# Optimization experiments

Hardware: AMD Instinct MI355X
Metric: run time of the kernel (lower is better)

The kernel has to match this reference:

```python
import jax, jax.numpy as jnp
import numpy as np

SEQ, B, N_IN, H, L = 8192, 1, 64, 1024, 5


def leaky_relu(x):
    return jnp.where(x >= 0, x, 0.01 * x)  # torch LeakyReLU default slope 0.01


def setup_inputs() -> dict:
    key = jax.random.key(0)
    ks = jax.random.split(key, 6)
    s_in = 1.0 / np.sqrt(N_IN)
    s_h = 1.0 / np.sqrt(H)
    return {
        "data_in": jax.random.normal(ks[0], (SEQ, B, N_IN), jnp.float32),
        "w1": jax.random.normal(ks[1], (H, N_IN), jnp.float32) * s_in,
        "b1": jnp.zeros((H,), jnp.float32),
        "W_ih": jax.random.normal(ks[2], (L, 4 * H, H), jnp.float32) * s_h,
        "W_hh": jax.random.normal(ks[3], (L, 4 * H, H), jnp.float32) * s_h,
        "b_ih": jnp.zeros((L, 4 * H), jnp.float32),
        "b_hh": jnp.zeros((L, 4 * H), jnp.float32),
        "w2": jax.random.normal(ks[4], (N_IN, H), jnp.float32) * s_h,
        "b2": jnp.zeros((N_IN,), jnp.float32),
        "h0": jnp.zeros((L, B, H), jnp.float32),
        "c0": jnp.zeros((L, B, H), jnp.float32),
    }


def _lstm_layer(x, h0, c0, Wih, Whh, b):
    # x: (SEQ, B, H_in); h0, c0: (B, H); Wih: (4H, H_in); Whh: (4H, H); b: (4H,)
    def step(carry, x_t):
        h, c = carry
        z = x_t @ Wih.T + h @ Whh.T + b  # (B, 4H)
        i, f, g, o = jnp.split(z, 4, axis=-1)  # torch gate order i,f,g,o
        i = jax.nn.sigmoid(i)
        f = jax.nn.sigmoid(f)
        g = jnp.tanh(g)
        o = jax.nn.sigmoid(o)
        c = f * c + i * g
        h = o * jnp.tanh(c)
        return (h, c), h

    (_, _), hs = jax.lax.scan(step, (h0, c0), x)
    return hs  # (SEQ, B, H)


def reference(data_in, w1, b1, W_ih, W_hh, b_ih, b_hh, w2, b2, h0, c0):
    out = leaky_relu(data_in @ w1.T + b1)  # (SEQ, B, H)
    for l in range(W_ih.shape[0]):  # stacked LSTM, layers is a static small int
        out = _lstm_layer(out, h0[l], c0[l], W_ih[l], W_hh[l], b_ih[l] + b_hh[l])
    out = leaky_relu(out)
    return jnp.tanh(out @ w2.T + b2)  # (SEQ, B, N_IN)
```

## Files before the change

### kernel.cpp

```cpp
#include <hip/hip_runtime.h>
#include <stdint.h>

typedef unsigned int  u32;
typedef unsigned short u16;

#define SEQ    8192
#define HID    1024
#define NL     5
#define NWG    256
#define TPB    256
#define PAIRS  20
#define RPW    20
#define NVR    12
#define NLR    8
#define WSTEPS (SEQ + NL - 1)
#define LWGS   52
#define RING   8

#define WS_X0    ((size_t)0)
#define WS_H5    ((size_t)16*1024*1024)
#define WS_SLOT  ((size_t)32*1024*1024)
#define WS_SYNC  (WS_SLOT + (size_t)128*1024)
#define WS_NEED  (WS_SYNC + 4096)

__device__ __forceinline__ float bf2f(u16 v) { return __uint_as_float(((u32)v) << 16); }
__device__ __forceinline__ float bflo(u32 v) { return __uint_as_float(v << 16); }
__device__ __forceinline__ float bfhi(u32 v) { return __uint_as_float(v & 0xffff0000u); }

__device__ __forceinline__ u16 f2bf(float f) {
  u32 u = __float_as_uint(f);
  u32 r = u + 0x7fffu + ((u >> 16) & 1u);
  return (u16)(r >> 16);
}
__device__ __forceinline__ float lrelu(float x) { return (x >= 0.f) ? x : 0.01f * x; }
__device__ __forceinline__ float sigm(float x)  { return 1.f / (1.f + __expf(-x)); }
__device__ __forceinline__ float tanh_f(float x) {
  float e = __expf(-2.f * fabsf(x));
  float t = (1.f - e) / (1.f + e);
  return (x >= 0.f) ? t : -t;
}

__device__ __forceinline__ float dot2bf(u32 w, u32 v, float acc) {
  return fmaf(bfhi(w), bfhi(v), fmaf(bflo(w), bflo(v), acc));
}

#if defined(__has_builtin)
#if __has_builtin(__builtin_amdgcn_fdot2_f32_bf16)
#define HAS_DOT2 1
typedef __bf16 bf16x2 __attribute__((ext_vector_type(2)));
__device__ __forceinline__ float hwdot2(u32 a, u32 b, float c) {
  union U { u32 u; bf16x2 v; };
  U x, y; x.u = a; y.u = b;
  return __builtin_amdgcn_fdot2_f32_bf16(x.v, y.v, c, false);
}
#endif
#endif
#ifndef HAS_DOT2
#define HAS_DOT2 0
__device__ __forceinline__ float hwdot2(u32 a, u32 b, float c) { return dot2bf(a, b, c); }
#endif

__device__ __forceinline__ u32 agent_load(const u32* p) {
  return __hip_atomic_load((u32*)p, __ATOMIC_RELAXED, __HIP_MEMORY_SCOPE_AGENT);
}
__device__ __forceinline__ void agent_store(u32* p, u32 v) {
  __hip_atomic_store(p, v, __ATOMIC_RELAXED, __HIP_MEMORY_SCOPE_AGENT);
}

__device__ __forceinline__ void rel_drain() {
  asm volatile("s_waitcnt vmcnt(0)" ::: "memory");
}

__device__ __forceinline__ int first_wg(int l) { return (l << 10) / PAIRS; }

__global__ void k_detect(const u32* __restrict__ w1, u32* __restrict__ flag) {
  int lane = threadIdx.x;
  int cnt = 0;
#pragma unroll
  for (int i = 0; i < 4; ++i) {
    u32 w = w1[lane * 4 + i];
    u32 e = (w >> 23) & 0xffu;
    cnt += (e >= 100u && e <= 140u) ? 1 : 0;
  }
  cnt += __shfl_xor(cnt, 32); cnt += __shfl_xor(cnt, 16); cnt += __shfl_xor(cnt, 8);
  cnt += __shfl_xor(cnt, 4);  cnt += __shfl_xor(cnt, 2);  cnt += __shfl_xor(cnt, 1);
  if (lane == 0) {
    u32 f = (cnt > 128) ? 1u : 0u;
#if HAS_DOT2
    u32 a1 = (u32)f2bf(1.5f)   | ((u32)f2bf(-2.25f) << 16);
    u32 b1v = (u32)f2bf(0.5f)  | ((u32)f2bf(4.0f)   << 16);
    u32 a2 = (u32)f2bf(0.125f) | ((u32)f2bf(3.0f)   << 16);
    u32 b2v = (u32)f2bf(8.0f)  | ((u32)f2bf(-0.5f)  << 16);
    float t1 = hwdot2(a1, b1v, 1.0f);
    float t2 = hwdot2(a2, b2v, 0.5f);
    if (fabsf(t1 + 7.25f) < 1e-2f && fabsf(t2) < 1e-2f) f |= 2u;
#endif
    *flag = f;
  }
}

__global__ void __launch_bounds__(256) k_in(const void* __restrict__ din,
                                            const void* __restrict__ w1,
                                            const void* __restrict__ b1,
                                            u32* __restrict__ X0,
                                            const u32* __restrict__ flagp) {
  const u32 isf = *flagp & 1u;
  int t = blockIdx.x, tid = threadIdx.x;
  __shared__ float xs[64];
  if (isf) {
    if (tid < 64) xs[tid] = ((const float*)din)[(size_t)t * 64 + tid];
  } else {
    if (tid < 32) {
      u32 v = ((const u32*)din)[(size_t)t * 32 + tid];
      xs[2 * tid] = bflo(v); xs[2 * tid + 1] = bfhi(v);
    }
  }
  __syncthreads();
  float o[4];
#pragma unroll
  for (int r = 0; r < 4; ++r) {
    int i = tid * 4 + r;
    float a = 0.f;
    if (isf) {
      const float* wr = (const float*)w1 + (size_t)i * 64;
#pragma unroll
      for (int d = 0; d < 64; ++d) a = fmaf(wr[d], xs[d], a);
      a += ((const float*)b1)[i];
    } else {
      const u32* wr = (const u32*)w1 + (size_t)i * 32;
#pragma unroll
      for (int d = 0; d < 32; ++d) {
        u32 w = wr[d];
        a = fmaf(bflo(w), xs[2 * d], a);
        a = fmaf(bfhi(w), xs[2 * d + 1], a);
      }
      a += bf2f(((const u16*)b1)[i]);
    }
    o[r] = lrelu(a);
  }
  X0[(size_t)t * 512 + tid * 2]     = (u32)f2bf(o[0]) | ((u32)f2bf(o[1]) << 16);
  X0[(size_t)t * 512 + tid * 2 + 1] = (u32)f2bf(o[2]) | ((u32)f2bf(o[3]) << 16);
}

__global__ void __launch_bounds__(TPB, 1) k_wave(const void* __restrict__ WihP,
                                                 const void* __restrict__ WhhP,
                                                 const void* __restrict__ bihP,
                                                 const void* __restrict__ bhhP,
                                                 const void* __restrict__ h0P,
                                                 const void* __restrict__ c0P,
                                                 const u32* __restrict__ X0,
                                                 u32* __restrict__ H5,
                                                 u32* slots, u32* flags,
                                                 const u32* __restrict__ flagp) {
  const u32 dfl = *flagp;
  const u32 isf = dfl & 1u;
  const bool ud2 = (dfl & 2u) != 0u;
  const int tid  = threadIdx.x;
  const int lane = tid & 63;
  const int wv   = tid >> 6;
  const int wg   = blockIdx.x;

  __shared__ u32   vlds[2][64 * 17];
  __shared__ u32   wlds[4 * NLR * 1024];
  __shared__ float zrow[80];

  u32 W[NVR][16];
#pragma unroll
  for (int i = 0; i < RPW; ++i) {
    int rr = wv * RPW + i;
    int p = rr >> 2, q = rr & 3;
    int g = wg * PAIRS + p;
    int lg = g >> 10, j = g & 1023;
    u32 tmp[16];
    if (isf) {
      const float* matf = (lane < 32) ? (const float*)WihP : (const float*)WhhP;
      const float4* s4 = (const float4*)(matf + ((size_t)(lg * 4096 + q * 1024 + j)) * 1024 + (lane & 31) * 32);
#pragma unroll
      for (int q4 = 0; q4 < 8; ++q4) {
        float4 f = s4[q4];
        tmp[q4 * 2]     = (u32)f2bf(f.x) | ((u32)f2bf(f.y) << 16);
        tmp[q4 * 2 + 1] = (u32)f2bf(f.z) | ((u32)f2bf(f.w) << 16);
      }
    } else {
      const u32* mat = (lane < 32) ? (const u32*)WihP : (const u32*)WhhP;
      const uint4* s4 = (const uint4*)(mat + ((size_t)(lg * 4096 + q * 1024 + j)) * 512 + (lane & 31) * 16);
      uint4 a0 = s4[0], a1 = s4[1], a2 = s4[2], a3 = s4[3];
      tmp[0]=a0.x; tmp[1]=a0.y; tmp[2]=a0.z;  tmp[3]=a0.w;
      tmp[4]=a1.x; tmp[5]=a1.y; tmp[6]=a1.z;  tmp[7]=a1.w;
      tmp[8]=a2.x; tmp[9]=a2.y; tmp[10]=a2.z; tmp[11]=a2.w;
      tmp[12]=a3.x;tmp[13]=a3.y;tmp[14]=a3.z; tmp[15]=a3.w;
    }
    if (i < NVR) {
#pragma unroll
      for (int d = 0; d < 16; ++d) W[i][d] = tmp[d];
    } else {
      u32* base = &wlds[(wv * NLR + (i - NVR)) * 1024];
#pragma unroll
      for (int d4 = 0; d4 < 4; ++d4) {
        uint4 v4 = make_uint4(tmp[d4*4], tmp[d4*4+1], tmp[d4*4+2], tmp[d4*4+3]);
        *(uint4*)&base[d4 * 256 + lane * 4] = v4;
      }
    }
  }

  float cst = 0.f;
  float b0 = 0.f, b1g = 0.f, b2g = 0.f, b3g = 0.f;
  if (wv == 0 && lane < PAIRS) {
    int g = wg * PAIRS + lane, lg = g >> 10, j = g & 1023;
    cst = isf ? ((const float*)c0P)[lg * 1024 + j] : bf2f(((const u16*)c0P)[lg * 1024 + j]);
#pragma unroll
    for (int q = 0; q < 4; ++q) {
      int r = lg * 4096 + q * 1024 + j;
      float bb = isf ? (((const float*)bihP)[r] + ((const float*)bhhP)[r])
                     : (bf2f(((const u16*)bihP)[r]) + bf2f(((const u16*)bhhP)[r]));
      if (q == 0) b0 = bb; else if (q == 1) b1g = bb; else if (q == 2) b2g = bb; else b3g = bb;
    }
  }
  if (tid < PAIRS / 2) {
    int g = wg * PAIRS + 2 * tid, lg = g >> 10, j = g & 1023;
    u32 v;
    if (isf) {
      const float* h0f = (const float*)h0P;
      v = (u32)f2bf(h0f[lg * 1024 + j]) | ((u32)f2bf(h0f[lg * 1024 + j + 1]) << 16);
    } else {
      const u16* h0b = (const u16*)h0P;
      v = (u32)h0b[lg * 1024 + j] | ((u32)h0b[lg * 1024 + j + 1] << 16);
    }
    agent_store(&slots[(size_t)(lg * RING + 7) * 512 + (j >> 1)], v);
  }

  const int l_lo = (wg * PAIRS) >> 10;
  const int l_hi = (wg * PAIRS + PAIRS - 1) >> 10;
  const int mlo = (l_lo > 0) ? l_lo - 1 : 0;
  const bool haswar = (l_hi + 1) < NL;
  const int f_lo = first_wg(l_lo), f_hi = first_wg(l_hi);

  __threadfence();
  __syncthreads();
  if (tid == 0) {
    agent_store(&flags[l_lo * 64 + (wg - f_lo)], 1u);
    if (l_hi != l_lo) agent_store(&flags[l_hi * 64 + (wg - f_hi)], 1u);
  }

  int budget = 20000000;

  for (int s = 0; s < WSTEPS; ++s) {
    if (wv == 0) {
      u32 need = (u32)(s + 1);
      for (;;) {
        u32 mn = 0xFFFFFFFFu;
        if (lane < LWGS) {
          for (int m = mlo; m <= l_hi; ++m) {
            u32 v = agent_load(&flags[m * 64 + lane]);
            mn = (v < mn) ? v : mn;
          }
          if (haswar) {
            u32 v = agent_load(&flags[(l_hi + 1) * 64 + lane]) + (u32)(RING - 2);
            mn = (v < mn) ? v : mn;
          }
        }
        u32 o;
        o = (u32)__shfl_xor((int)mn, 32); mn = (o < mn) ? o : mn;
        o = (u32)__shfl_xor((int)mn, 16); mn = (o < mn) ? o : mn;
        o = (u32)__shfl_xor((int)mn, 8);  mn = (o < mn) ? o : mn;
        o = (u32)__shfl_xor((int)mn, 4);  mn = (o < mn) ? o : mn;
        o = (u32)__shfl_xor((int)mn, 2);  mn = (o < mn) ? o : mn;
        o = (u32)__shfl_xor((int)mn, 1);  mn = (o < mn) ? o : mn;
        if (mn >= need) break;
        if (--budget < 0) break;
      }
    }
    __syncthreads();

#pragma unroll
    for (int sel = 0; sel < 2; ++sel) {
      int L = l_lo + sel;
      if (L <= l_hi) {
        int t = s - L;
        if (t >= 0 && t < SEQ) {
          const u32* hsrc = slots + (size_t)(L * RING + ((t - 1) & 7)) * 512;
          const u32* xsrc = (L == 0) ? (X0 + (size_t)t * 512)
                                     : (slots + (size_t)((L - 1) * RING + (t & 7)) * 512);
#pragma unroll
          for (int rr2 = 0; rr2 < 4; ++rr2) {
            int gidx = tid + rr2 * 256;
            u32 val;
            if (gidx < 512) val = (L == 0) ? xsrc[gidx] : agent_load(&xsrc[gidx]);
            else            val = agent_load(&hsrc[gidx - 512]);
            vlds[sel][(gidx >> 4) * 17 + (gidx & 15)] = val;
          }
        }
      }
    }
    __syncthreads();

    {
      int curl = -1;
      u32 vreg[16];
#pragma unroll
      for (int i = 0; i < RPW; ++i) {
        int rr = wv * RPW + i;
        int p = rr >> 2;
        int g = wg * PAIRS + p;
        int lg = g >> 10;
        int t = s - lg;
        if (t >= 0 && t < SEQ) {
          if (lg != curl) {
            curl = lg;
            const u32* vb = &vlds[lg - l_lo][lane * 17];
#pragma unroll
            for (int d = 0; d < 16; ++d) vreg[d] = vb[d];
          }
          float a0 = 0.f, a1 = 0.f, a2 = 0.f, a3 = 0.f;
          if (i < NVR) {
            if (ud2) {
#pragma unroll
              for (int d = 0; d < 16; d += 4) {
                a0 = hwdot2(W[i][d],   vreg[d],   a0);
                a1 = hwdot2(W[i][d+1], vreg[d+1], a1);
                a2 = hwdot2(W[i][d+2], vreg[d+2], a2);
                a3 = hwdot2(W[i][d+3], vreg[d+3], a3);
              }
            } else {
#pragma unroll
              for (int d = 0; d < 16; d += 4) {
                a0 = fmaf(bflo(W[i][d]),   bflo(vreg[d]),   a0);
                a0 = fmaf(bfhi(W[i][d]),   bfhi(vreg[d]),   a0);
                a1 = fmaf(bflo(W[i][d+1]), bflo(vreg[d+1]), a1);
                a1 = fmaf(bfhi(W[i][d+1]), bfhi(vreg[d+1]), a1);
                a2 = fmaf(bflo(W[i][d+2]), bflo(vreg[d+2]), a2);
                a2 = fmaf(bfhi(W[i][d+2]), bfhi(vreg[d+2]), a2);
                a3 = fmaf(bflo(W[i][d+3]), bflo(vreg[d+3]), a3);
                a3 = fmaf(bfhi(W[i][d+3]), bfhi(vreg[d+3]), a3);
              }
            }
          } else {
            const uint4* wl = (const uint4*)&wlds[(wv * NLR + (i - NVR)) * 1024 + lane * 4];
#pragma unroll
            for (int d4 = 0; d4 < 4; ++d4) {
              uint4 w4 = wl[d4 * 64];
              if (ud2) {
                a0 = hwdot2(w4.x, vreg[d4*4+0], a0);
                a1 = hwdot2(w4.y, vreg[d4*4+1], a1);
                a2 = hwdot2(w4.z, vreg[d4*4+2], a2);
                a3 = hwdot2(w4.w, vreg[d4*4+3], a3);
              } else {
                a0 = fmaf(bflo(w4.x), bflo(vreg[d4*4+0]), a0);
                a0 = fmaf(bfhi(w4.x), bfhi(vreg[d4*4+0]), a0);
                a1 = fmaf(bflo(w4.y), bflo(vreg[d4*4+1]), a1);
                a1 = fmaf(bfhi(w4.y), bfhi(vreg[d4*4+1]), a1);
                a2 = fmaf(bflo(w4.z), bflo(vreg[d4*4+2]), a2);
                a2 = fmaf(bfhi(w4.z), bfhi(vreg[d4*4+2]), a2);
                a3 = fmaf(bflo(w4.w), bflo(vreg[d4*4+3]), a3);
                a3 = fmaf(bfhi(w4.w), bfhi(vreg[d4*4+3]), a3);
              }
            }
          }
          float r = (a0 + a1) + (a2 + a3);
          r += __shfl_xor(r, 32);
          r += __shfl_xor(r, 16);
          r += __shfl_xor(r, 8);
          r += __shfl_xor(r, 4);
          r += __shfl_xor(r, 2);
          r += __shfl_xor(r, 1);
          if (lane == 0) zrow[rr] = r;
        }
      }
    }
    __syncthreads();

    if (wv == 0) {
      u16 hb = 0;
      int g = wg * PAIRS + lane;
      int lg = g >> 10;
      int t = s - lg;
      bool act = (lane < PAIRS) && (t >= 0) && (t < SEQ);
      if (act) {
        float zi = zrow[lane * 4 + 0] + b0;
        float zf = zrow[lane * 4 + 1] + b1g;
        float zg = zrow[lane * 4 + 2] + b2g;
        float zo = zrow[lane * 4 + 3] + b3g;
        float ig = sigm(zi), fg = sigm(zf), gg = tanh_f(zg), og = sigm(zo);
        float c = fg * cst + ig * gg;
        cst = c;
        hb = f2bf(og * tanh_f(c));
      }
      u16 hnb = (u16)__shfl_xor((int)hb, 1);
      if (act && ((lane & 1) == 0)) {
        int j = g & 1023;
        u32 v = (u32)hb | ((u32)hnb << 16);
        agent_store(&slots[(size_t)(lg * RING + (t & 7)) * 512 + (j >> 1)], v);
        if (lg == NL - 1) H5[(size_t)t * 512 + (j >> 1)] = v;
      }
      rel_drain();
      if (lane == 0) {
        agent_store(&flags[l_lo * 64 + (wg - f_lo)], (u32)(s + 2));
        if (l_hi != l_lo) agent_store(&flags[l_hi * 64 + (wg - f_hi)], (u32)(s + 2));
      }
    }
  }
}

__global__ void __launch_bounds__(256) k_out(const u32* __restrict__ H5,
                                             const void* __restrict__ w2,
                                             const void* __restrict__ b2,
                                             void* __restrict__ out,
                                             const u32* __restrict__ flagp) {
  const u32 isf = *flagp & 1u;
  int t = blockIdx.x, tid = threadIdx.x;
  __shared__ float hs[1024];
  __shared__ float part[256];
#pragma unroll
  for (int r = 0; r < 2; ++r) {
    int idx = tid + r * 256;
    u32 v = H5[(size_t)t * 512 + idx];
    hs[2 * idx]     = lrelu(bflo(v));
    hs[2 * idx + 1] = lrelu(bfhi(v));
  }
  __syncthreads();
  int n = tid & 63, qq = tid >> 6;
  float a = 0.f;
  if (isf) {
    const float* wr = (const float*)w2 + (size_t)n * 1024 + qq * 256;
    const float* hb = &hs[qq * 256];
#pragma unroll
    for (int d = 0; d < 256; ++d) a = fmaf(wr[d], hb[d], a);
  } else {
    const u32* wr = (const u32*)w2 + (size_t)n * 512 + qq * 128;
    const float* hb = &hs[qq * 256];
#pragma unroll
    for (int d = 0; d < 128; ++d) {
      u32 w = wr[d];
      a = fmaf(bflo(w), hb[2 * d], a);
      a = fmaf(bfhi(w), hb[2 * d + 1], a);
    }
  }
  part[tid] = a;
  __syncthreads();
  if (tid < 64) {
    float bb = isf ? ((const float*)b2)[tid] : bf2f(((const u16*)b2)[tid]);
    float y = part[tid] + part[tid + 64] + part[tid + 128] + part[tid + 192] + bb;
    float r = tanh_f(y);
    if (isf) ((float*)out)[(size_t)t * 64 + tid] = r;
    else     ((u16*)out)[(size_t)t * 64 + tid] = f2bf(r);
  }
}

extern "C" void kernel_launch(void* const* d_in, const int* in_sizes, int n_in,
                              void* d_out, int out_size, void* d_ws, size_t ws_size,
                              hipStream_t stream) {
  (void)in_sizes; (void)n_in; (void)out_size;
  if (ws_size < WS_NEED) return;

  const void* din = d_in[0];
  const void* w1  = d_in[1];
  const void* b1  = d_in[2];
  const void* Wih = d_in[3];
  const void* Whh = d_in[4];
  const void* bih = d_in[5];
  const void* bhh = d_in[6];
  const void* w2  = d_in[7];
  const void* b2  = d_in[8];
  const void* h0  = d_in[9];
  const void* c0  = d_in[10];

  char* ws = (char*)d_ws;
  u32* X0    = (u32*)(ws + WS_X0);
  u32* H5    = (u32*)(ws + WS_H5);
  u32* slot  = (u32*)(ws + WS_SLOT);
  u32* flags = (u32*)(ws + WS_SYNC);
  u32* dflag = (u32*)(ws + WS_SYNC + 2048);

  hipMemsetAsync(flags, 0, 4096, stream);
  k_detect<<<1, 64, 0, stream>>>((const u32*)w1, dflag);
  k_in  <<<SEQ, 256, 0, stream>>>(din, w1, b1, X0, dflag);
  k_wave<<<NWG, TPB, 0, stream>>>(Wih, Whh, bih, bhh, h0, c0, X0, H5, slot, flags, dflag);
  k_out <<<SEQ, 256, 0, stream>>>(H5, w2, b2, d_out, dflag);
}
```

Measured before the change: 116.4 ms.

## Replace flag-based step sync with sequence-tagged data chunks in LSTM wavefront

Hidden-state ring slots now hold per-workgroup 16-word chunks, each 4-word group carrying a timestep tag next to three data words. Consumers poll the tags of the chunks they need instead of a separate flag array. This removes the separate flag store, the vmcnt drain and the flag-then-data round trip on every step. Stores go out as dwordx4 with sc0 sc1 so each tag and its data arrive together at the last-level cache. The cost is index arithmetic (divide by ten, padding) in the gather, wider polling loads, and a write-after-read flag that is still kept for ring reuse.

```diff
diff --git a/kernel.cpp b/kernel.cpp
--- a/kernel.cpp
+++ b/kernel.cpp
@@ -16,11 +16,13 @@
 #define WSTEPS (SEQ + NL - 1)
 #define LWGS   52
 #define RING   8
+#define CHW    16
+#define SSTR   (LWGS * CHW)
 
 #define WS_X0    ((size_t)0)
 #define WS_H5    ((size_t)16*1024*1024)
 #define WS_SLOT  ((size_t)32*1024*1024)
-#define WS_SYNC  (WS_SLOT + (size_t)128*1024)
+#define WS_SYNC  (WS_SLOT + (size_t)192*1024)
 #define WS_NEED  (WS_SYNC + 4096)
 
 __device__ __forceinline__ float bf2f(u16 v) { return __uint_as_float(((u32)v) << 16); }
@@ -63,15 +65,19 @@
 __device__ __forceinline__ u32 agent_load(const u32* p) {
   return __hip_atomic_load((u32*)p, __ATOMIC_RELAXED, __HIP_MEMORY_SCOPE_AGENT);
 }
-__device__ __forceinline__ void agent_store(u32* p, u32 v) {
-  __hip_atomic_store(p, v, __ATOMIC_RELAXED, __HIP_MEMORY_SCOPE_AGENT);
-}
-
-__device__ __forceinline__ void rel_drain() {
-  asm volatile("s_waitcnt vmcnt(0)" ::: "memory");
+
+__device__ __forceinline__ void llc_store(u32* p, u32 v) {
+  asm volatile("global_store_dword %0, %1, off sc0 sc1" : : "v"(p), "v"(v) : "memory");
+}
+
+typedef u32 u32x4_t __attribute__((ext_vector_type(4)));
+__device__ __forceinline__ void llc_store4(u32* p, u32 tag, u32 a, u32 b, u32 c) {
+  u32x4_t q; q.x = tag; q.y = a; q.z = b; q.w = c;
+  asm volatile("global_store_dwordx4 %0, %1, off sc0 sc1" : : "v"(p), "v"(q) : "memory");
 }
 
 __device__ __forceinline__ int first_wg(int l) { return (l << 10) / PAIRS; }
+
 
 __global__ void k_detect(const u32* __restrict__ w1, u32* __restrict__ flag) {
   int lane = threadIdx.x;
@@ -216,57 +222,78 @@
       if (q == 0) b0 = bb; else if (q == 1) b1g = bb; else if (q == 2) b2g = bb; else b3g = bb;
     }
   }
-  if (tid < PAIRS / 2) {
-    int g = wg * PAIRS + 2 * tid, lg = g >> 10, j = g & 1023;
-    u32 v;
-    if (isf) {
-      const float* h0f = (const float*)h0P;
-      v = (u32)f2bf(h0f[lg * 1024 + j]) | ((u32)f2bf(h0f[lg * 1024 + j + 1]) << 16);
-    } else {
-      const u16* h0b = (const u16*)h0P;
-      v = (u32)h0b[lg * 1024 + j] | ((u32)h0b[lg * 1024 + j + 1] << 16);
-    }
-    agent_store(&slots[(size_t)(lg * RING + 7) * 512 + (j >> 1)], v);
-  }
 
   const int l_lo = (wg * PAIRS) >> 10;
   const int l_hi = (wg * PAIRS + PAIRS - 1) >> 10;
-  const int mlo = (l_lo > 0) ? l_lo - 1 : 0;
-  const bool haswar = (l_hi + 1) < NL;
+  const bool span = (l_hi != l_lo);
   const int f_lo = first_wg(l_lo), f_hi = first_wg(l_hi);
-
-  __threadfence();
+  const int c_lo = wg - f_lo, c_hi = wg - f_hi;
+
+  if (wv == 0) {
+    int g = wg * PAIRS + lane;
+    int lg = g >> 10, j = g & 1023;
+    u32 hv = 0;
+    if ((lane < PAIRS) && !(lane & 1)) {
+      if (isf) {
+        const float* h0f = (const float*)h0P;
+        hv = (u32)f2bf(h0f[lg * 1024 + j]) | ((u32)f2bf(h0f[lg * 1024 + j + 1]) << 16);
+      } else {
+        const u16* h0b = (const u16*)h0P;
+        hv = (u32)h0b[lg * 1024 + j] | ((u32)h0b[lg * 1024 + j + 1] << 16);
+      }
+    }
+    u32 ga = (u32)__shfl((int)hv, 6 * (lane & 3));
+    u32 gb = (u32)__shfl((int)hv, 6 * (lane & 3) + 2);
+    u32 gc = (u32)__shfl((int)hv, 6 * (lane & 3) + 4);
+#pragma unroll
+    for (int sel = 0; sel < 2; ++sel) {
+      int L = l_lo + sel;
+      if (L <= l_hi) {
+        int cc = (sel == 0) ? c_lo : c_hi;
+        u32* cb = slots + (L * RING + 7) * SSTR + cc * CHW;
+        if (lane < 4) llc_store4(cb + lane * 4, 0xFFFFFFFFu, ga, gb, gc);
+      }
+    }
+  }
   __syncthreads();
-  if (tid == 0) {
-    agent_store(&flags[l_lo * 64 + (wg - f_lo)], 1u);
-    if (l_hi != l_lo) agent_store(&flags[l_hi * 64 + (wg - f_hi)], 1u);
-  }
 
   int budget = 20000000;
 
   for (int s = 0; s < WSTEPS; ++s) {
+    const int t0 = s - l_lo;
+    const int t1 = s - l_hi;
+    if (t1 >= SEQ) break;
+    const bool p0 = (t0 >= 0) && (t0 < SEQ);
+    const bool p1 = span && (t1 >= 0);
+
     if (wv == 0) {
-      u32 need = (u32)(s + 1);
+      const u32 need = (u32)(s + 1);
+      const int lc = lane * CHW;
+      const u32 *tA = 0, *tXA = 0, *tB = 0, *tXB = 0, *wf1 = 0, *wf2 = 0;
+      u32 eA = 0, eXA = 0, eB = 0, eXB = 0;
+      if (p0) { tA = slots + (l_lo * RING + ((t0 - 1) & 7)) * SSTR + lc; eA = (u32)(t0 - 1); }
+      if (p0 && l_lo > 0) { tXA = slots + ((l_lo - 1) * RING + (t0 & 7)) * SSTR + lc; eXA = (u32)t0; }
+      if (p1) {
+        tB  = slots + (l_hi * RING + ((t1 - 1) & 7)) * SSTR + lc; eB  = (u32)(t1 - 1);
+        tXB = slots + (l_lo * RING + (t1 & 7)) * SSTR + lc;       eXB = (u32)t1;
+      }
+      if (p0 && (l_lo + 1) < NL)         wf1 = flags + (l_lo + 1) * 64 + lane;
+      if (span && p1 && (l_hi + 1) < NL) wf2 = flags + (l_hi + 1) * 64 + lane;
       for (;;) {
-        u32 mn = 0xFFFFFFFFu;
+        bool pass = true;
         if (lane < LWGS) {
-          for (int m = mlo; m <= l_hi; ++m) {
-            u32 v = agent_load(&flags[m * 64 + lane]);
-            mn = (v < mn) ? v : mn;
-          }
-          if (haswar) {
-            u32 v = agent_load(&flags[(l_hi + 1) * 64 + lane]) + (u32)(RING - 2);
-            mn = (v < mn) ? v : mn;
-          }
+          if (tA)  pass = pass & (agent_load(tA)  == eA)  & (agent_load(tA + 4)  == eA)
+                               & (agent_load(tA + 8)  == eA)  & (agent_load(tA + 12)  == eA);
+          if (tXA) pass = pass & (agent_load(tXA) == eXA) & (agent_load(tXA + 4) == eXA)
+                               & (agent_load(tXA + 8) == eXA) & (agent_load(tXA + 12) == eXA);
+          if (tB)  pass = pass & (agent_load(tB)  == eB)  & (agent_load(tB + 4)  == eB)
+                               & (agent_load(tB + 8)  == eB)  & (agent_load(tB + 12)  == eB);
+          if (tXB) pass = pass & (agent_load(tXB) == eXB) & (agent_load(tXB + 4) == eXB)
+                               & (agent_load(tXB + 8) == eXB) & (agent_load(tXB + 12) == eXB);
+          if (wf1) pass = pass & ((agent_load(wf1) + (u32)(RING - 2)) >= need);
+          if (wf2) pass = pass & ((agent_load(wf2) + (u32)(RING - 2)) >= need);
         }
-        u32 o;
-        o = (u32)__shfl_xor((int)mn, 32); mn = (o < mn) ? o : mn;
-        o = (u32)__shfl_xor((int)mn, 16); mn = (o < mn) ? o : mn;
-        o = (u32)__shfl_xor((int)mn, 8);  mn = (o < mn) ? o : mn;
-        o = (u32)__shfl_xor((int)mn, 4);  mn = (o < mn) ? o : mn;
-        o = (u32)__shfl_xor((int)mn, 2);  mn = (o < mn) ? o : mn;
-        o = (u32)__shfl_xor((int)mn, 1);  mn = (o < mn) ? o : mn;
-        if (mn >= need) break;
+        if (__all(pass)) break;
         if (--budget < 0) break;
       }
     }
@@ -278,15 +305,29 @@
       if (L <= l_hi) {
         int t = s - L;
         if (t >= 0 && t < SEQ) {
-          const u32* hsrc = slots + (size_t)(L * RING + ((t - 1) & 7)) * 512;
-          const u32* xsrc = (L == 0) ? (X0 + (size_t)t * 512)
-                                     : (slots + (size_t)((L - 1) * RING + (t & 7)) * 512);
 #pragma unroll
           for (int rr2 = 0; rr2 < 4; ++rr2) {
             int gidx = tid + rr2 * 256;
             u32 val;
-            if (gidx < 512) val = (L == 0) ? xsrc[gidx] : agent_load(&xsrc[gidx]);
-            else            val = agent_load(&hsrc[gidx - 512]);
+            if (gidx < 512) {
+              if (L == 0) {
+                val = X0[(size_t)t * 512 + gidx];
+              } else {
+                int qp = (L - 1) * 512 + gidx;
+                int wsrc = (qp * 6554) >> 16;
+                int qq = qp - wsrc * 10;
+                int word = 1 + qq + ((qq * 11) >> 5);
+                val = agent_load(slots + ((L - 1) * RING + (t & 7)) * SSTR
+                                 + (wsrc - first_wg(L - 1)) * CHW + word);
+              }
+            } else {
+              int qp = L * 512 + (gidx - 512);
+              int wsrc = (qp * 6554) >> 16;
+              int qq = qp - wsrc * 10;
+              int word = 1 + qq + ((qq * 11) >> 5);
+              val = agent_load(slots + (L * RING + ((t - 1) & 7)) * SSTR
+                               + (wsrc - first_wg(L)) * CHW + word);
+            }
             vlds[sel][(gidx >> 4) * 17 + (gidx & 15)] = val;
           }
         }
@@ -373,8 +414,8 @@
       u16 hb = 0;
       int g = wg * PAIRS + lane;
       int lg = g >> 10;
-      int t = s - lg;
-      bool act = (lane < PAIRS) && (t >= 0) && (t < SEQ);
+      int tg = s - lg;
+      bool act = (lane < PAIRS) && (tg >= 0) && (tg < SEQ);
       if (act) {
         float zi = zrow[lane * 4 + 0] + b0;
         float zf = zrow[lane * 4 + 1] + b1g;
@@ -386,16 +427,27 @@
         hb = f2bf(og * tanh_f(c));
       }
       u16 hnb = (u16)__shfl_xor((int)hb, 1);
-      if (act && ((lane & 1) == 0)) {
-        int j = g & 1023;
-        u32 v = (u32)hb | ((u32)hnb << 16);
-        agent_store(&slots[(size_t)(lg * RING + (t & 7)) * 512 + (j >> 1)], v);
-        if (lg == NL - 1) H5[(size_t)t * 512 + (j >> 1)] = v;
-      }
-      rel_drain();
+      u32 v = (u32)hb | ((u32)hnb << 16);
+      u32 ga = (u32)__shfl((int)v, 6 * (lane & 3));
+      u32 gb = (u32)__shfl((int)v, 6 * (lane & 3) + 2);
+      u32 gc = (u32)__shfl((int)v, 6 * (lane & 3) + 4);
+#pragma unroll
+      for (int sel = 0; sel < 2; ++sel) {
+        int L = l_lo + sel;
+        if (L <= l_hi) {
+          int tL = s - L;
+          if (tL >= 0 && tL < SEQ) {
+            int cc = (sel == 0) ? c_lo : c_hi;
+            u32* cb = slots + (L * RING + (tL & 7)) * SSTR + cc * CHW;
+            if (lane < 4) llc_store4(cb + lane * 4, (u32)tL, ga, gb, gc);
+            if (act && !(lane & 1) && (lg == L) && (L == NL - 1))
+              H5[(size_t)tL * 512 + ((g & 1023) >> 1)] = v;
+          }
+        }
+      }
       if (lane == 0) {
-        agent_store(&flags[l_lo * 64 + (wg - f_lo)], (u32)(s + 2));
-        if (l_hi != l_lo) agent_store(&flags[l_hi * 64 + (wg - f_hi)], (u32)(s + 2));
+        if (l_lo > 0) llc_store(flags + l_lo * 64 + c_lo, (u32)(s + 2));
+        if (span)     llc_store(flags + l_hi * 64 + c_hi, (u32)(s + 2));
       }
     }
   }
```

Result: slower. 127.0 ms (+9.1%).

## Replace flag-polling barrier with sequence-tagged slots and per-layer epoch counters

Applied to the files above, without the earlier changes.

Each hidden-state slot entry becomes a 64-bit word holding the bf16 pair and its timestep tag, so consumers spin directly on the data until the tags match. This replaces the per-step min-reduction over all producer flags and the vmcnt drain before publishing. Write-after-read safety now uses per-layer atomic epoch counters, checked only against the next layer, and the ring is deepened to 16 slots. The slot area doubles in size and epoch updates are contended atomics, and correctness depends on 64-bit atomic stores landing as one unit.

```diff
diff --git a/kernel.cpp b/kernel.cpp
--- a/kernel.cpp
+++ b/kernel.cpp
@@ -3,6 +3,7 @@
 
 typedef unsigned int  u32;
 typedef unsigned short u16;
+typedef unsigned long long u64;
 
 #define SEQ    8192
 #define HID    1024
@@ -15,12 +16,12 @@
 #define NLR    8
 #define WSTEPS (SEQ + NL - 1)
 #define LWGS   52
-#define RING   8
+#define RING   16
 
 #define WS_X0    ((size_t)0)
 #define WS_H5    ((size_t)16*1024*1024)
 #define WS_SLOT  ((size_t)32*1024*1024)
-#define WS_SYNC  (WS_SLOT + (size_t)128*1024)
+#define WS_SYNC  (WS_SLOT + (size_t)384*1024)
 #define WS_NEED  (WS_SYNC + 4096)
 
 __device__ __forceinline__ float bf2f(u16 v) { return __uint_as_float(((u32)v) << 16); }
@@ -63,15 +64,15 @@
 __device__ __forceinline__ u32 agent_load(const u32* p) {
   return __hip_atomic_load((u32*)p, __ATOMIC_RELAXED, __HIP_MEMORY_SCOPE_AGENT);
 }
-__device__ __forceinline__ void agent_store(u32* p, u32 v) {
+__device__ __forceinline__ u64 slot_load(const u64* p) {
+  return __hip_atomic_load((u64*)p, __ATOMIC_RELAXED, __HIP_MEMORY_SCOPE_AGENT);
+}
+__device__ __forceinline__ void slot_store(u64* p, u64 v) {
   __hip_atomic_store(p, v, __ATOMIC_RELAXED, __HIP_MEMORY_SCOPE_AGENT);
 }
-
-__device__ __forceinline__ void rel_drain() {
-  asm volatile("s_waitcnt vmcnt(0)" ::: "memory");
-}
-
-__device__ __forceinline__ int first_wg(int l) { return (l << 10) / PAIRS; }
+__device__ __forceinline__ void epoch_add(u32* p) {
+  (void)__hip_atomic_fetch_add(p, 1u, __ATOMIC_RELAXED, __HIP_MEMORY_SCOPE_AGENT);
+}
 
 __global__ void k_detect(const u32* __restrict__ w1, u32* __restrict__ flag) {
   int lane = threadIdx.x;
@@ -150,7 +151,7 @@
                                                  const void* __restrict__ c0P,
                                                  const u32* __restrict__ X0,
                                                  u32* __restrict__ H5,
-                                                 u32* slots, u32* flags,
+                                                 u64* slots64, u32* epochs,
                                                  const u32* __restrict__ flagp) {
   const u32 dfl = *flagp;
   const u32 isf = dfl & 1u;
@@ -226,68 +227,55 @@
       const u16* h0b = (const u16*)h0P;
       v = (u32)h0b[lg * 1024 + j] | ((u32)h0b[lg * 1024 + j + 1] << 16);
     }
-    agent_store(&slots[(size_t)(lg * RING + 7) * 512 + (j >> 1)], v);
+    slot_store(&slots64[(size_t)(lg * RING + (RING - 1)) * 512 + (j >> 1)],
+               ((u64)0xFFFFFFFFull << 32) | (u64)v);
   }
 
   const int l_lo = (wg * PAIRS) >> 10;
   const int l_hi = (wg * PAIRS + PAIRS - 1) >> 10;
-  const int mlo = (l_lo > 0) ? l_lo - 1 : 0;
-  const bool haswar = (l_hi + 1) < NL;
-  const int f_lo = first_wg(l_lo), f_hi = first_wg(l_hi);
-
-  __threadfence();
-  __syncthreads();
-  if (tid == 0) {
-    agent_store(&flags[l_lo * 64 + (wg - f_lo)], 1u);
-    if (l_hi != l_lo) agent_store(&flags[l_hi * 64 + (wg - f_hi)], 1u);
-  }
 
   int budget = 20000000;
 
   for (int s = 0; s < WSTEPS; ++s) {
-    if (wv == 0) {
-      u32 need = (u32)(s + 1);
-      for (;;) {
-        u32 mn = 0xFFFFFFFFu;
-        if (lane < LWGS) {
-          for (int m = mlo; m <= l_hi; ++m) {
-            u32 v = agent_load(&flags[m * 64 + lane]);
-            mn = (v < mn) ? v : mn;
-          }
-          if (haswar) {
-            u32 v = agent_load(&flags[(l_hi + 1) * 64 + lane]) + (u32)(RING - 2);
-            mn = (v < mn) ? v : mn;
-          }
-        }
-        u32 o;
-        o = (u32)__shfl_xor((int)mn, 32); mn = (o < mn) ? o : mn;
-        o = (u32)__shfl_xor((int)mn, 16); mn = (o < mn) ? o : mn;
-        o = (u32)__shfl_xor((int)mn, 8);  mn = (o < mn) ? o : mn;
-        o = (u32)__shfl_xor((int)mn, 4);  mn = (o < mn) ? o : mn;
-        o = (u32)__shfl_xor((int)mn, 2);  mn = (o < mn) ? o : mn;
-        o = (u32)__shfl_xor((int)mn, 1);  mn = (o < mn) ? o : mn;
-        if (mn >= need) break;
-        if (--budget < 0) break;
-      }
-    }
-    __syncthreads();
-
 #pragma unroll
     for (int sel = 0; sel < 2; ++sel) {
       int L = l_lo + sel;
       if (L <= l_hi) {
         int t = s - L;
         if (t >= 0 && t < SEQ) {
-          const u32* hsrc = slots + (size_t)(L * RING + ((t - 1) & 7)) * 512;
-          const u32* xsrc = (L == 0) ? (X0 + (size_t)t * 512)
-                                     : (slots + (size_t)((L - 1) * RING + (t & 7)) * 512);
+          const u64* hsrc = slots64 + (size_t)(L * RING + ((t - 1) & (RING - 1))) * 512;
+          const u64* xsrc = (L > 0) ? slots64 + (size_t)((L - 1) * RING + (t & (RING - 1))) * 512
+                                    : (const u64*)0;
+          const u32 exph = (u32)(t - 1);
+          const u32 expx = (u32)t;
+          u32 okm = 0;
+          u32 dat[4] = {0u, 0u, 0u, 0u};
+          int miss = 0;
+          for (;;) {
+#pragma unroll
+            for (int rr2 = 0; rr2 < 4; ++rr2) {
+              if (!(okm & (1u << rr2))) {
+                int gidx = tid + rr2 * 256;
+                if (gidx < 512) {
+                  if (L == 0) { dat[rr2] = X0[(size_t)t * 512 + gidx]; okm |= 1u << rr2; }
+                  else {
+                    u64 v = slot_load(xsrc + gidx);
+                    if ((u32)(v >> 32) == expx) { dat[rr2] = (u32)v; okm |= 1u << rr2; }
+                  }
+                } else {
+                  u64 v = slot_load(hsrc + (gidx - 512));
+                  if ((u32)(v >> 32) == exph) { dat[rr2] = (u32)v; okm |= 1u << rr2; }
+                }
+              }
+            }
+            if (__all(okm == 15u)) break;
+            if (--budget < 0) break;
+            if (++miss >= 16) __builtin_amdgcn_s_sleep(1);
+          }
 #pragma unroll
           for (int rr2 = 0; rr2 < 4; ++rr2) {
             int gidx = tid + rr2 * 256;
-            u32 val;
-            if (gidx < 512) val = (L == 0) ? xsrc[gidx] : agent_load(&xsrc[gidx]);
-            else            val = agent_load(&hsrc[gidx - 512]);
-            vlds[sel][(gidx >> 4) * 17 + (gidx & 15)] = val;
+            vlds[sel][(gidx >> 4) * 17 + (gidx & 15)] = dat[rr2];
           }
         }
       }
@@ -370,6 +358,22 @@
     __syncthreads();
 
     if (wv == 0) {
+      if (s >= RING - 1) {
+        u32 needw = 52u * (u32)(s - (RING - 2));
+#pragma unroll
+        for (int sel = 0; sel < 2; ++sel) {
+          int L = l_lo + sel;
+          if (L <= l_hi && (L + 1) < NL) {
+            int tL = s - L;
+            if (tL >= 0 && tL < SEQ) {
+              while (agent_load(&epochs[(L + 1) * 32]) < needw) {
+                if (--budget < 0) break;
+                __builtin_amdgcn_s_sleep(4);
+              }
+            }
+          }
+        }
+      }
       u16 hb = 0;
       int g = wg * PAIRS + lane;
       int lg = g >> 10;
@@ -389,13 +393,13 @@
       if (act && ((lane & 1) == 0)) {
         int j = g & 1023;
         u32 v = (u32)hb | ((u32)hnb << 16);
-        agent_store(&slots[(size_t)(lg * RING + (t & 7)) * 512 + (j >> 1)], v);
+        slot_store(&slots64[(size_t)(lg * RING + (t & (RING - 1))) * 512 + (j >> 1)],
+                   ((u64)(u32)t << 32) | (u64)v);
         if (lg == NL - 1) H5[(size_t)t * 512 + (j >> 1)] = v;
       }
-      rel_drain();
       if (lane == 0) {
-        agent_store(&flags[l_lo * 64 + (wg - f_lo)], (u32)(s + 2));
-        if (l_hi != l_lo) agent_store(&flags[l_hi * 64 + (wg - f_hi)], (u32)(s + 2));
+        epoch_add(&epochs[l_lo * 32]);
+        if (l_hi != l_lo) epoch_add(&epochs[l_hi * 32]);
       }
     }
   }
@@ -465,15 +469,16 @@
   const void* c0  = d_in[10];
 
   char* ws = (char*)d_ws;
-  u32* X0    = (u32*)(ws + WS_X0);
-  u32* H5    = (u32*)(ws + WS_H5);
-  u32* slot  = (u32*)(ws + WS_SLOT);
-  u32* flags = (u32*)(ws + WS_SYNC);
-  u32* dflag = (u32*)(ws + WS_SYNC + 2048);
-
-  hipMemsetAsync(flags, 0, 4096, stream);
+  u32* X0     = (u32*)(ws + WS_X0);
+  u32* H5     = (u32*)(ws + WS_H5);
+  u64* slot   = (u64*)(ws + WS_SLOT);
+  u32* epochs = (u32*)(ws + WS_SYNC);
+  u32* dflag  = (u32*)(ws + WS_SYNC + 2048);
+
+  hipMemsetAsync(slot, 0xAA, (size_t)NL * RING * 512 * 8, stream);
+  hipMemsetAsync(epochs, 0, 4096, stream);
   k_detect<<<1, 64, 0, stream>>>((const u32*)w1, dflag);
   k_in  <<<SEQ, 256, 0, stream>>>(din, w1, b1, X0, dflag);
-  k_wave<<<NWG, TPB, 0, stream>>>(Wih, Whh, bih, bhh, h0, c0, X0, H5, slot, flags, dflag);
+  k_wave<<<NWG, TPB, 0, stream>>>(Wih, Whh, bih, bhh, h0, c0, X0, H5, slot, epochs, dflag);
   k_out <<<SEQ, 256, 0, stream>>>(H5, w2, b2, d_out, dflag);
 }
```

Result: faster. 103.6 ms (-11.0%).
